# Optimization experiments

Measured on AMD Instinct MI355X. Metric: run time of the kernel, lower is better.

## Reference

```python
import jax, jax.numpy as jnp
import numpy as np

B, N, E = 2, 2048, 1024
H, D = 16, 64  # context_dim = H*D = 1024


def setup_inputs() -> dict:
    key = jax.random.key(0)
    ks = jax.random.split(key, 6)
    s = 0.02
    return {
        "input_emb": jax.random.normal(ks[0], (B, N, E), dtype=jnp.float32),
        "Wq": jax.random.normal(ks[1], (E, H * D), dtype=jnp.float32) * s,
        "Wk": jax.random.normal(ks[2], (E, D), dtype=jnp.float32) * s,
        "Wv": jax.random.normal(ks[3], (E, D), dtype=jnp.float32) * s,
        "Wo": jax.random.normal(ks[4], (H * D, H * D), dtype=jnp.float32) * s,
        "bo": jax.random.normal(ks[5], (H * D,), dtype=jnp.float32) * s,
    }


def reference(input_emb, Wq, Wk, Wv, Wo, bo):
    b, n, _ = input_emb.shape
    Q = (input_emb @ Wq).reshape(b, n, H, D)          # (B,N,H,D)
    K = input_emb @ Wk                                 # (B,N,D) shared across heads (MQA)
    V = input_emb @ Wv                                 # (B,N,D)
    # scores: (B,H,N,N); mask is applied before scaling in the torch code,
    # but -inf/scale == -inf so mask-then-scale == scale-then-mask.
    scores = jnp.einsum("bnhd,bmd->bhnm", Q, K) / jnp.sqrt(jnp.float32(D))
    causal = jnp.tril(jnp.ones((n, n), dtype=bool))    # True = keep
    scores = jnp.where(causal[None, None], scores, -jnp.inf)
    weights = jax.nn.softmax(scores, axis=-1)          # dropout rate 0.0 -> identity
    Z = jnp.einsum("bhnm,bmd->bnhd", weights, V).reshape(b, n, H * D)
    return Z @ Wo + bo
```

## Files before the change

### kernel.cpp

```cpp
#include <hip/hip_runtime.h>
#include <hip/hip_bf16.h>


#define NQ 2048
#define BATCH 2
#define HEADS 16
#define HD 64
#define EMB 1024
#define NKV 1152

typedef short s16x8 __attribute__((ext_vector_type(8)));
typedef float f32x4 __attribute__((ext_vector_type(4)));
typedef unsigned int u32x4 __attribute__((ext_vector_type(4)));
typedef unsigned short ushort_t;

__device__ __forceinline__ ushort_t f2bf(float f) {
    unsigned u = __builtin_bit_cast(unsigned, f);
    u += 0x7fff + ((u >> 16) & 1);
    return (ushort_t)(u >> 16);
}

__device__ __forceinline__ void store_out(float* p, float v) { *p = v; }
__device__ __forceinline__ void store_out(ushort_t* p, float v) { *p = f2bf(v); }

#define GL16(g, l)                                                                  \
    __builtin_amdgcn_global_load_lds(                                               \
        (const __attribute__((address_space(1))) unsigned int*)(g),                 \
        (__attribute__((address_space(3))) unsigned int*)(l), 16, 0, 0)

__global__ __launch_bounds__(256) void prep(const float* __restrict__ x,
                                            const float* __restrict__ Wq,
                                            const float* __restrict__ Wk,
                                            const float* __restrict__ Wv,
                                            const float* __restrict__ Wo,
                                            ushort_t* __restrict__ xb,
                                            ushort_t* __restrict__ Wqkv_t,
                                            ushort_t* __restrict__ Wo_t) {
    const int bid = blockIdx.x, t = threadIdx.x;
    if (bid < 4096) {
        const int i = bid * 1024 + t * 4;
        const float4 v = *(const float4*)&x[i];
        ushort_t o[4] = {f2bf(v.x), f2bf(v.y), f2bf(v.z), f2bf(v.w)};
        *(uint2*)&xb[i] = *(uint2*)o;
        return;
    }
    int tb = bid - 4096;
    const float* src; ushort_t* dst; int N, n0, k0;
    if (tb < 1024)      { src = Wq; N = 1024; dst = Wqkv_t;
                          n0 = (tb & 31) * 32; k0 = (tb >> 5) * 32; }
    else if (tb < 1088) { tb -= 1024; src = Wk; N = 64; dst = Wqkv_t + (size_t)1024 * EMB;
                          n0 = (tb & 1) * 32; k0 = (tb >> 1) * 32; }
    else if (tb < 1152) { tb -= 1088; src = Wv; N = 64; dst = Wqkv_t + (size_t)1088 * EMB;
                          n0 = (tb & 1) * 32; k0 = (tb >> 1) * 32; }
    else                { tb -= 1152; src = Wo; N = 1024; dst = Wo_t;
                          n0 = (tb & 31) * 32; k0 = (tb >> 5) * 32; }
    __shared__ float tile[32][33];
    const int tx = t & 31, ty = t >> 5;
#pragma unroll
    for (int i = 0; i < 32; i += 8)
        tile[ty + i][tx] = src[(size_t)(k0 + ty + i) * N + n0 + tx];
    __syncthreads();
#pragma unroll
    for (int i = 0; i < 32; i += 8)
        dst[(size_t)(n0 + ty + i) * EMB + k0 + tx] = f2bf(tile[tx][ty + i]);
}

__device__ __forceinline__ s16x8 frag(const ushort_t* lds, int row, int lc) {
    const int phys = lc ^ (row & 7);
    return *(const s16x8*)&lds[row * 64 + phys * 8];
}

template<bool HAS_BIAS, bool WRITE_VT, typename OutT>
__global__ __launch_bounds__(256, 2) void gemm_bf16(const ushort_t* __restrict__ A,
                                                    const ushort_t* __restrict__ Bt,
                                                    const float* __restrict__ bias,
                                                    OutT* __restrict__ C,
                                                    ushort_t* __restrict__ Vt,
                                                    int M, int N, int K) {
    __shared__ __align__(16) ushort_t Al[2][128 * 64];
    __shared__ __align__(16) ushort_t Bl[2][128 * 64];
    const int t = threadIdx.x;
    const int w = t >> 6, lane = t & 63, quad = lane >> 4, ln = lane & 15;
    const int wm = w >> 1, wn = w & 1;

    const int nwg = gridDim.x * gridDim.y;
    int lin = blockIdx.y * gridDim.x + blockIdx.x;
    lin = (lin & 7) * (nwg >> 3) + (lin >> 3);
    const int bx = lin % gridDim.x, by = lin / gridDim.x;
    const int row0 = by * 128, col0 = bx * 128;

    const ushort_t* pA[4];
    const ushort_t* pB[4];
#pragma unroll
    for (int it = 0; it < 4; ++it) {
        const int u = (w * 4 + it) * 64 + lane;
        const int row = u >> 3, pc = u & 7;
        const int lc = pc ^ (row & 7);
        pA[it] = A + (size_t)(row0 + row) * K + lc * 8;
        pB[it] = Bt + (size_t)(col0 + row) * K + lc * 8;
    }

#define STAGE_AB(la, lb)                                                            \
    {                                                                               \
        _Pragma("unroll")                                                           \
        for (int it = 0; it < 4; ++it) {                                            \
            GL16(pA[it], (la) + (w * 4 + it) * 512);                                \
            GL16(pB[it], (lb) + (w * 4 + it) * 512);                                \
            pA[it] += 64;                                                           \
            pB[it] += 64;                                                           \
        }                                                                           \
    }

    f32x4 acc[4][4] = {};
    const int nk = K >> 6;

    STAGE_AB(Al[0], Bl[0]);
    __syncthreads();

#pragma unroll 1
    for (int ks = 0; ks < nk; ++ks) {
        const int cur = ks & 1;
        if (ks + 1 < nk) STAGE_AB(Al[cur ^ 1], Bl[cur ^ 1]);

        const ushort_t* la = Al[cur];
        const ushort_t* lb = Bl[cur];
        s16x8 af[4][2], bf[4][2];
#pragma unroll
        for (int mt = 0; mt < 4; ++mt) {
            af[mt][0] = frag(la, wm * 64 + mt * 16 + ln, quad);
            af[mt][1] = frag(la, wm * 64 + mt * 16 + ln, 4 + quad);
        }
#pragma unroll
        for (int nt = 0; nt < 4; ++nt) {
            bf[nt][0] = frag(lb, wn * 64 + nt * 16 + ln, quad);
            bf[nt][1] = frag(lb, wn * 64 + nt * 16 + ln, 4 + quad);
        }
#pragma unroll
        for (int mt = 0; mt < 4; ++mt)
#pragma unroll
            for (int nt = 0; nt < 4; ++nt) {
                acc[mt][nt] = __builtin_amdgcn_mfma_f32_16x16x32_bf16(
                    af[mt][0], bf[nt][0], acc[mt][nt], 0, 0, 0);
                acc[mt][nt] = __builtin_amdgcn_mfma_f32_16x16x32_bf16(
                    af[mt][1], bf[nt][1], acc[mt][nt], 0, 0, 0);
            }
        __syncthreads();
    }
#undef STAGE_AB

#pragma unroll
    for (int nt = 0; nt < 4; ++nt) {
        const int col = col0 + wn * 64 + nt * 16 + ln;
        const float bv = HAS_BIAS ? bias[col] : 0.f;
#pragma unroll
        for (int mt = 0; mt < 4; ++mt) {
#pragma unroll
            for (int r = 0; r < 4; ++r) {
                const int row = row0 + wm * 64 + mt * 16 + quad * 4 + r;
                float v = acc[mt][nt][r] + bv;
                if (WRITE_VT && col < 1024) v *= 0.18033688011112043f;
                store_out(&C[(size_t)row * N + col], v);
            }
            if (WRITE_VT && col >= 1088) {
                const int d = col - 1088;
                const int n = row0 + wm * 64 + mt * 16 + quad * 4;
                const int bb = n >> 11, nn = n & 2047;
                ushort_t tmp[4] = {f2bf(acc[mt][nt][0]), f2bf(acc[mt][nt][1]),
                                   f2bf(acc[mt][nt][2]), f2bf(acc[mt][nt][3])};
                *(uint2*)&Vt[((size_t)bb * 64 + d) * NQ + nn] = *(uint2*)tmp;
            }
        }
    }
}

__device__ __forceinline__ void stage_tile(ushort_t* lds, const ushort_t* g,
                                           size_t rstride, int w, int lane) {
#pragma unroll
    for (int it = 0; it < 2; ++it) {
        const int u = (w * 2 + it) * 64 + lane;
        const int row = u >> 3, pc = u & 7;
        const int lc = pc ^ (row & 7);
        GL16(g + (size_t)row * rstride + lc * 8, lds + (size_t)(w * 2 + it) * 512);
    }
}

__device__ __forceinline__ void stage_k(ushort_t* lds, const ushort_t* g,
                                        int w, int lane) {
#pragma unroll
    for (int it = 0; it < 2; ++it) {
        const int u = (w * 2 + it) * 64 + lane;
        const int row = u >> 3, pc = u & 7;
        const int lc = pc ^ (row & 7);
        const int grow = (row & 32) | (((row >> 2) & 3) << 3) |
                         (((row >> 4) & 1) << 2) | (row & 3);
        GL16(g + (size_t)grow * NKV + lc * 8, lds + (size_t)(w * 2 + it) * 512);
    }
}

__global__ __launch_bounds__(256, 2) void attn_mfma(const ushort_t* __restrict__ QKV,
                                                    const ushort_t* __restrict__ Vt,
                                                    ushort_t* __restrict__ Z) {
    const int bid = blockIdx.x;
    const int g = bid & 7, u = bid >> 3;
    const int hg = u & 3, tt = u >> 2;
    const int ib = g + 8 * tt;
    const int b = ib & 1, iq = ib >> 1;
    const int m = (iq < 32) ? iq : 95 - iq;
    const int iters = (m >> 1) + 1;
    const int qbase = m * 32;

    const int t = threadIdx.x;
    const int w = t >> 6, lane = t & 63, quad = lane >> 4, ln = lane & 15;
    const int h = hg * 4 + w;

    __shared__ __align__(16) ushort_t Kl[2][64 * 64];
    __shared__ __align__(16) ushort_t Vl[2][64 * 64];

    const ushort_t* Kg = QKV + (size_t)b * NQ * NKV + 1024;
    const ushort_t* Vg = Vt + (size_t)b * 64 * NQ;

    s16x8 aQ[2][2];
#pragma unroll
    for (int ss = 0; ss < 2; ++ss) {
        const ushort_t* Qg =
            QKV + (size_t)(b * NQ + qbase + ss * 16 + ln) * NKV + h * HD;
        aQ[ss][0] = *(const s16x8*)(Qg + quad * 8);
        aQ[ss][1] = *(const s16x8*)(Qg + 32 + quad * 8);
    }

    stage_k(Kl[0], Kg, w, lane);
    stage_tile(Vl[0], Vg, NQ, w, lane);
    __syncthreads();

    f32x4 o[2][4];
#pragma unroll
    for (int ss = 0; ss < 2; ++ss)
#pragma unroll
        for (int ii = 0; ii < 4; ++ii) o[ss][ii] = f32x4{0.f, 0.f, 0.f, 0.f};
    float mrow[2] = {-1e30f, -1e30f}, lrow[2] = {0.f, 0.f};

#pragma unroll 1
    for (int jt = 0; jt < iters; ++jt) {
        const int cur = jt & 1;
        if (jt + 1 < iters) {
            stage_k(Kl[cur ^ 1], Kg + (size_t)(jt + 1) * 64 * NKV, w, lane);
            stage_tile(Vl[cur ^ 1], Vg + (jt + 1) * 64, NQ, w, lane);
        }
        const ushort_t* Kc = Kl[cur];
        const ushort_t* Vc = Vl[cur];

        s16x8 kf0[4], kf1[4];
#pragma unroll
        for (int nt = 0; nt < 4; ++nt) {
            kf0[nt] = frag(Kc, nt * 16 + ln, quad);
            kf1[nt] = frag(Kc, nt * 16 + ln, 4 + quad);
        }

        f32x4 sx[2][4];
        __builtin_amdgcn_s_setprio(1);
#pragma unroll
        for (int ss = 0; ss < 2; ++ss)
#pragma unroll
            for (int nt = 0; nt < 4; ++nt) {
                f32x4 acc = f32x4{0.f, 0.f, 0.f, 0.f};
                acc = __builtin_amdgcn_mfma_f32_16x16x32_bf16(kf0[nt], aQ[ss][0],
                                                              acc, 0, 0, 0);
                acc = __builtin_amdgcn_mfma_f32_16x16x32_bf16(kf1[nt], aQ[ss][1],
                                                              acc, 0, 0, 0);
                sx[ss][nt] = acc;
            }
        __builtin_amdgcn_s_setprio(0);

        s16x8 vf0[4], vf1[4];
#pragma unroll
        for (int nt = 0; nt < 4; ++nt) {
            vf0[nt] = frag(Vc, nt * 16 + ln, quad);
            vf1[nt] = frag(Vc, nt * 16 + ln, 4 + quad);
        }

        if (jt == iters - 1) {
#pragma unroll
            for (int ss = 0; ss < 2; ++ss) {
                const int qa = qbase + ss * 16 + ln;
#pragma unroll
                for (int nt = 0; nt < 4; ++nt)
#pragma unroll
                    for (int r = 0; r < 4; ++r) {
                        const int kv =
                            jt * 64 + (nt >> 1) * 32 + quad * 8 + (nt & 1) * 4 + r;
                        if (kv > qa) sx[ss][nt][r] = -1e30f;
                    }
            }
        }

        unsigned bp0[2][4], bp1[2][4];
#pragma unroll
        for (int ss = 0; ss < 2; ++ss) {
            const float r0 = fmaxf(fmaxf(sx[ss][0][0], sx[ss][0][1]),
                                   fmaxf(sx[ss][0][2], sx[ss][0][3]));
            const float r1 = fmaxf(fmaxf(sx[ss][1][0], sx[ss][1][1]),
                                   fmaxf(sx[ss][1][2], sx[ss][1][3]));
            const float r2 = fmaxf(fmaxf(sx[ss][2][0], sx[ss][2][1]),
                                   fmaxf(sx[ss][2][2], sx[ss][2][3]));
            const float r3 = fmaxf(fmaxf(sx[ss][3][0], sx[ss][3][1]),
                                   fmaxf(sx[ss][3][2], sx[ss][3][3]));
            float rmax = fmaxf(fmaxf(r0, r1), fmaxf(r2, r3));
            rmax = fmaxf(rmax, __shfl_xor(rmax, 16));
            rmax = fmaxf(rmax, __shfl_xor(rmax, 32));

            if (!__all(rmax - mrow[ss] <= 8.f)) {
                const float mnew = fmaxf(mrow[ss], rmax);
                const float al = __builtin_amdgcn_exp2f(mrow[ss] - mnew);
                mrow[ss] = mnew;
                lrow[ss] *= al;
#pragma unroll
                for (int ntd = 0; ntd < 4; ++ntd)
#pragma unroll
                    for (int r = 0; r < 4; ++r) o[ss][ntd][r] *= al;
            }

            float rsum = 0.f;
#pragma unroll
            for (int nt = 0; nt < 4; ++nt)
#pragma unroll
                for (int r = 0; r < 4; ++r) {
                    const float pv = __builtin_amdgcn_exp2f(sx[ss][nt][r] - mrow[ss]);
                    sx[ss][nt][r] = pv;
                    rsum += pv;
                }
            rsum += __shfl_xor(rsum, 16);
            rsum += __shfl_xor(rsum, 32);
            lrow[ss] += rsum;

#pragma unroll
            for (int jj = 0; jj < 4; ++jj) {
                const int nt0 = jj >> 1, rr = 2 * (jj & 1);
                asm("v_cvt_pk_bf16_f32 %0, %1, %2"
                    : "=v"(bp0[ss][jj])
                    : "v"(sx[ss][nt0][rr]), "v"(sx[ss][nt0][rr + 1]));
                asm("v_cvt_pk_bf16_f32 %0, %1, %2"
                    : "=v"(bp1[ss][jj])
                    : "v"(sx[ss][2 + nt0][rr]), "v"(sx[ss][2 + nt0][rr + 1]));
            }
        }

        __builtin_amdgcn_s_setprio(1);
#pragma unroll
        for (int ss = 0; ss < 2; ++ss) {
            const s16x8 bP0 = __builtin_bit_cast(
                s16x8, u32x4{bp0[ss][0], bp0[ss][1], bp0[ss][2], bp0[ss][3]});
            const s16x8 bP1 = __builtin_bit_cast(
                s16x8, u32x4{bp1[ss][0], bp1[ss][1], bp1[ss][2], bp1[ss][3]});
#pragma unroll
            for (int ntd = 0; ntd < 4; ++ntd) {
                o[ss][ntd] = __builtin_amdgcn_mfma_f32_16x16x32_bf16(
                    vf0[ntd], bP0, o[ss][ntd], 0, 0, 0);
                o[ss][ntd] = __builtin_amdgcn_mfma_f32_16x16x32_bf16(
                    vf1[ntd], bP1, o[ss][ntd], 0, 0, 0);
            }
        }
        __builtin_amdgcn_s_setprio(0);
        __syncthreads();
    }

#pragma unroll
    for (int ss = 0; ss < 2; ++ss) {
        const float invl = 1.f / lrow[ss];
        const size_t row = (size_t)(b * NQ + qbase + ss * 16 + ln);
#pragma unroll
        for (int ntd = 0; ntd < 4; ++ntd) {
            ushort_t tmp[4];
#pragma unroll
            for (int r = 0; r < 4; ++r) tmp[r] = f2bf(o[ss][ntd][r] * invl);
            *(uint2*)&Z[row * EMB + h * HD + ntd * 16 + quad * 4] = *(uint2*)tmp;
        }
    }
}

extern "C" void kernel_launch(void* const* d_in, const int* in_sizes, int n_in,
                              void* d_out, int out_size, void* d_ws, size_t ws_size,
                              hipStream_t stream) {
    const float* x  = (const float*)d_in[0];
    const float* Wq = (const float*)d_in[1];
    const float* Wk = (const float*)d_in[2];
    const float* Wv = (const float*)d_in[3];
    const float* Wo = (const float*)d_in[4];
    const float* bo = (const float*)d_in[5];
    float* out = (float*)d_out;

    const int M = BATCH * NQ;
    char* ws = (char*)d_ws;
    ushort_t* xb     = (ushort_t*)ws;
    ushort_t* Wqkv_t = (ushort_t*)(ws + (size_t)8  * 1024 * 1024);
    ushort_t* Wo_t   = (ushort_t*)(ws + (size_t)11 * 1024 * 1024);
    ushort_t* QKV    = (ushort_t*)(ws + (size_t)13 * 1024 * 1024);
    ushort_t* Vt     = (ushort_t*)(ws + (size_t)23 * 1024 * 1024);
    ushort_t* Zb     = (ushort_t*)(ws + (size_t)24 * 1024 * 1024);

    dim3 blk(256);
    prep<<<dim3(6272), blk, 0, stream>>>(x, Wq, Wk, Wv, Wo, xb, Wqkv_t, Wo_t);
    gemm_bf16<false, true, ushort_t><<<dim3(NKV / 128, M / 64 / 2), blk, 0, stream>>>(
        xb, Wqkv_t, nullptr, QKV, Vt, M, NKV, EMB);
    attn_mfma<<<dim3(512), blk, 0, stream>>>(QKV, Vt, Zb);
    gemm_bf16<true, false, float><<<dim3(EMB / 128, M / 64 / 2), blk, 0, stream>>>(
        Zb, Wo_t, bo, out, nullptr, M, EMB, EMB);
}
```

Measured before the change: 170.2 us.

## Split attention work per head with 2-wave blocks over 64-row query tiles

The attention kernel moves from 256-thread blocks, where four waves handle four heads for one 32-row query tile, to 128-thread blocks where two waves handle one head for a 64-row query tile, launched over 1024 blocks. The causal load-balancing order changes from pairing 32-row tiles to an interleaved ordering of 64-row tiles, and each wave now issues more staging loads. This is meant to improve occupancy and scheduling balance across CUs. In exchange, each K/V tile staged in LDS is shared by only one head instead of four, which increases global and LDS traffic per unit of compute.

```diff
diff --git a/kernel.cpp b/kernel.cpp
--- a/kernel.cpp
+++ b/kernel.cpp
@@ -173,45 +173,40 @@
     }
 }
 
-__device__ __forceinline__ void stage_tile(ushort_t* lds, const ushort_t* g,
-                                           size_t rstride, int w, int lane) {
-#pragma unroll
-    for (int it = 0; it < 2; ++it) {
-        const int u = (w * 2 + it) * 64 + lane;
+__device__ __forceinline__ void stage_tile2(ushort_t* lds, const ushort_t* g,
+                                            size_t rstride, int w, int lane) {
+#pragma unroll
+    for (int it = 0; it < 4; ++it) {
+        const int u = (w * 4 + it) * 64 + lane;
         const int row = u >> 3, pc = u & 7;
         const int lc = pc ^ (row & 7);
-        GL16(g + (size_t)row * rstride + lc * 8, lds + (size_t)(w * 2 + it) * 512);
-    }
-}
-
-__device__ __forceinline__ void stage_k(ushort_t* lds, const ushort_t* g,
-                                        int w, int lane) {
-#pragma unroll
-    for (int it = 0; it < 2; ++it) {
-        const int u = (w * 2 + it) * 64 + lane;
+        GL16(g + (size_t)row * rstride + lc * 8, lds + (size_t)(w * 4 + it) * 512);
+    }
+}
+
+__device__ __forceinline__ void stage_k2(ushort_t* lds, const ushort_t* g,
+                                         int w, int lane) {
+#pragma unroll
+    for (int it = 0; it < 4; ++it) {
+        const int u = (w * 4 + it) * 64 + lane;
         const int row = u >> 3, pc = u & 7;
         const int lc = pc ^ (row & 7);
         const int grow = (row & 32) | (((row >> 2) & 3) << 3) |
                          (((row >> 4) & 1) << 2) | (row & 3);
-        GL16(g + (size_t)grow * NKV + lc * 8, lds + (size_t)(w * 2 + it) * 512);
-    }
-}
-
-__global__ __launch_bounds__(256, 2) void attn_mfma(const ushort_t* __restrict__ QKV,
+        GL16(g + (size_t)grow * NKV + lc * 8, lds + (size_t)(w * 4 + it) * 512);
+    }
+}
+
+__global__ __launch_bounds__(128, 2) void attn_mfma(const ushort_t* __restrict__ QKV,
                                                     const ushort_t* __restrict__ Vt,
                                                     ushort_t* __restrict__ Z) {
     const int bid = blockIdx.x;
-    const int g = bid & 7, u = bid >> 3;
-    const int hg = u & 3, tt = u >> 2;
-    const int ib = g + 8 * tt;
-    const int b = ib & 1, iq = ib >> 1;
-    const int m = (iq < 32) ? iq : 95 - iq;
-    const int iters = (m >> 1) + 1;
-    const int qbase = m * 32;
-
+    const int b = (bid >> 4) & 1, h = bid & 15;
+    const int i = bid >> 5, k = i >> 3, j = i & 7;
+    const int qt = (k == 0) ? 2 * j : (k == 1) ? 31 - 2 * j
+                 : (k == 2) ? 2 * j + 1 : 30 - 2 * j;
     const int t = threadIdx.x;
     const int w = t >> 6, lane = t & 63, quad = lane >> 4, ln = lane & 15;
-    const int h = hg * 4 + w;
 
     __shared__ __align__(16) ushort_t Kl[2][64 * 64];
     __shared__ __align__(16) ushort_t Vl[2][64 * 64];
@@ -223,13 +218,13 @@
 #pragma unroll
     for (int ss = 0; ss < 2; ++ss) {
         const ushort_t* Qg =
-            QKV + (size_t)(b * NQ + qbase + ss * 16 + ln) * NKV + h * HD;
+            QKV + (size_t)(b * NQ + qt * 64 + w * 32 + ss * 16 + ln) * NKV + h * HD;
         aQ[ss][0] = *(const s16x8*)(Qg + quad * 8);
         aQ[ss][1] = *(const s16x8*)(Qg + 32 + quad * 8);
     }
 
-    stage_k(Kl[0], Kg, w, lane);
-    stage_tile(Vl[0], Vg, NQ, w, lane);
+    stage_k2(Kl[0], Kg, w, lane);
+    stage_tile2(Vl[0], Vg, NQ, w, lane);
     __syncthreads();
 
     f32x4 o[2][4];
@@ -240,11 +235,11 @@
     float mrow[2] = {-1e30f, -1e30f}, lrow[2] = {0.f, 0.f};
 
 #pragma unroll 1
-    for (int jt = 0; jt < iters; ++jt) {
+    for (int jt = 0; jt <= qt; ++jt) {
         const int cur = jt & 1;
-        if (jt + 1 < iters) {
-            stage_k(Kl[cur ^ 1], Kg + (size_t)(jt + 1) * 64 * NKV, w, lane);
-            stage_tile(Vl[cur ^ 1], Vg + (jt + 1) * 64, NQ, w, lane);
+        if (jt < qt) {
+            stage_k2(Kl[cur ^ 1], Kg + (size_t)(jt + 1) * 64 * NKV, w, lane);
+            stage_tile2(Vl[cur ^ 1], Vg + (jt + 1) * 64, NQ, w, lane);
         }
         const ushort_t* Kc = Kl[cur];
         const ushort_t* Vc = Vl[cur];
@@ -278,16 +273,15 @@
             vf1[nt] = frag(Vc, nt * 16 + ln, 4 + quad);
         }
 
-        if (jt == iters - 1) {
+        if (jt == qt) {
 #pragma unroll
             for (int ss = 0; ss < 2; ++ss) {
-                const int qa = qbase + ss * 16 + ln;
+                const int qa = w * 32 + ss * 16 + ln;
 #pragma unroll
                 for (int nt = 0; nt < 4; ++nt)
 #pragma unroll
                     for (int r = 0; r < 4; ++r) {
-                        const int kv =
-                            jt * 64 + (nt >> 1) * 32 + quad * 8 + (nt & 1) * 4 + r;
+                        const int kv = (nt >> 1) * 32 + quad * 8 + (nt & 1) * 4 + r;
                         if (kv > qa) sx[ss][nt][r] = -1e30f;
                     }
             }
@@ -366,7 +360,7 @@
 #pragma unroll
     for (int ss = 0; ss < 2; ++ss) {
         const float invl = 1.f / lrow[ss];
-        const size_t row = (size_t)(b * NQ + qbase + ss * 16 + ln);
+        const size_t row = (size_t)(b * NQ + qt * 64 + w * 32 + ss * 16 + ln);
 #pragma unroll
         for (int ntd = 0; ntd < 4; ++ntd) {
             ushort_t tmp[4];
@@ -397,11 +391,10 @@
     ushort_t* Vt     = (ushort_t*)(ws + (size_t)23 * 1024 * 1024);
     ushort_t* Zb     = (ushort_t*)(ws + (size_t)24 * 1024 * 1024);
 
-    dim3 blk(256);
-    prep<<<dim3(6272), blk, 0, stream>>>(x, Wq, Wk, Wv, Wo, xb, Wqkv_t, Wo_t);
-    gemm_bf16<false, true, ushort_t><<<dim3(NKV / 128, M / 64 / 2), blk, 0, stream>>>(
+    prep<<<dim3(6272), dim3(256), 0, stream>>>(x, Wq, Wk, Wv, Wo, xb, Wqkv_t, Wo_t);
+    gemm_bf16<false, true, ushort_t><<<dim3(NKV / 128, M / 128), dim3(256), 0, stream>>>(
         xb, Wqkv_t, nullptr, QKV, Vt, M, NKV, EMB);
-    attn_mfma<<<dim3(512), blk, 0, stream>>>(QKV, Vt, Zb);
-    gemm_bf16<true, false, float><<<dim3(EMB / 128, M / 64 / 2), blk, 0, stream>>>(
+    attn_mfma<<<dim3(1024), dim3(128), 0, stream>>>(QKV, Vt, Zb);
+    gemm_bf16<true, false, float><<<dim3(EMB / 128, M / 128), dim3(256), 0, stream>>>(
         Zb, Wo_t, bo, out, nullptr, M, EMB, EMB);
 }
```

Result: no change. 171.2 us (+0.6%).
